# Kernel tuning notes

Hardware: AMD Instinct MI355X
Metric: run time of the kernel (lower is better)

## Reference

```python
import jax, jax.numpy as jnp
import numpy as np
from jax import lax

INP = 512
OUT = 512
T = 2048
B = 64


def setup_inputs() -> dict:
    key = jax.random.key(0)
    ks = jax.random.split(key, 7)
    rang = (1.0 / OUT) ** 0.5
    u = lambda k, shape: jax.random.uniform(k, shape, jnp.float32, -rang, rang)
    return {
        "x": jax.random.normal(ks[0], (T, B, INP), jnp.float32),
        "g": u(ks[1], (INP, OUT)),
        "gb": u(ks[2], (OUT,)),
        "h": u(ks[3], (INP, OUT)),
        "hb": u(ks[4], (OUT,)),
        "r": u(ks[5], (1, OUT)),
        "rb": u(ks[6], (OUT,)),
    }


def reference(x, g, gb, h, hb, r, rb):
    # x: [T, B, inp]
    Tn = x.shape[0]
    # time gate: r_t = 2*sigmoid((n/T) * r + rb), shape [T, out]
    t = (jnp.arange(Tn, dtype=x.dtype) / Tn)[:, None]  # [T, 1]
    rt = 2.0 * jax.nn.sigmoid(t * r[0] + rb)           # [T, out]
    # precompute per-step gates (vectorized over T)
    G = jax.nn.sigmoid(jnp.einsum("tbi,io->tbo", x, g) + gb) * rt[:, None, :]
    H = jnp.tanh(jnp.einsum("tbi,io->tbo", x, h) + hb) * rt[:, None, :]

    def step(y, gh):
        g_t, h_t = gh
        return y * g_t + h_t, None

    y0 = jnp.zeros((x.shape[1], x.shape[2] * 0 + G.shape[-1]), dtype=x.dtype)
    y, _ = lax.scan(step, y0, (G, H))
    return y
```

## Files before the change

### kernel.cpp

```cpp
#include <hip/hip_runtime.h>
#include <cstdint>
#include <cstddef>

#define TT   2048
#define BB   64
#define KK   512
#define OO   512
#define NCH  64
#define TC   32

typedef __attribute__((ext_vector_type(8))) short short8;
typedef __attribute__((ext_vector_type(4))) float f32x4;

__device__ __forceinline__ unsigned short f2bf(float f) {
  unsigned int u = __float_as_uint(f);
  unsigned int rounding = 0x7FFFu + ((u >> 16) & 1u);
  return (unsigned short)((u + rounding) >> 16);
}

__device__ __forceinline__ float sigmoid_f(float z) {
  return 1.0f / (1.0f + __expf(-z));
}

__device__ __forceinline__ float tanh_f(float z) {
  z = fminf(15.0f, fmaxf(-15.0f, z));
  float e = __expf(-2.0f * z);
  return (1.0f - e) / (1.0f + e);
}

__device__ __forceinline__ void async_ld16(const void* g, void* l) {
  __builtin_amdgcn_global_load_lds(
      (const __attribute__((address_space(1))) void*)g,
      (__attribute__((address_space(3))) void*)l, 16, 0, 0);
}

__global__ void convert_x_k(const float4* __restrict__ x4,
                            ushort4* __restrict__ xb4, int n4) {
  int i = blockIdx.x * blockDim.x + threadIdx.x;
  int stride = gridDim.x * blockDim.x;
  for (; i < n4; i += stride) {
    float4 v = x4[i];
    ushort4 o;
    o.x = f2bf(v.x); o.y = f2bf(v.y); o.z = f2bf(v.z); o.w = f2bf(v.w);
    xb4[i] = o;
  }
}

__global__ void prep_weights_k(const float* __restrict__ g,
                               const float* __restrict__ h,
                               unsigned short* __restrict__ Gt,
                               unsigned short* __restrict__ Ht) {
  __shared__ float tile[32][33];
  const float* src = (blockIdx.z == 0) ? g : h;
  unsigned short* dst = (blockIdx.z == 0) ? Gt : Ht;
  int ox = blockIdx.x * 32;
  int ky = blockIdx.y * 32;
  int tx = threadIdx.x, ty = threadIdx.y;
  #pragma unroll
  for (int r = ty; r < 32; r += 8)
    tile[r][tx] = src[(ky + r) * OO + ox + tx];
  __syncthreads();
  #pragma unroll
  for (int r = ty; r < 32; r += 8)
    dst[(size_t)(ox + r) * KK + ky + tx] = f2bf(tile[tx][r]);
}

__global__ __launch_bounds__(512, 2) void rnn_fused3_k(
    const unsigned short* __restrict__ xb,
    const unsigned short* __restrict__ Gt,
    const unsigned short* __restrict__ Ht,
    const float* __restrict__ gb, const float* __restrict__ hb,
    const float* __restrict__ r,  const float* __restrict__ rb,
    float* __restrict__ chunkA, float* __restrict__ chunkB) {
  extern __shared__ __align__(16) unsigned short smem[];

  const int tid  = threadIdx.x;
  const int wave = tid >> 6;
  const int lane = tid & 63;
  const int quad = lane >> 4;
  const int lcol = lane & 15;

  const int bi = blockIdx.x;
  const int ot = bi >> 6;
  const int c  = bi & 63;
  const int o  = ot * 128 + wave * 16 + lcol;

  const float gbv = gb[o], hbv = hb[o];
  const float rv  = r[o],  rbv = rb[o];

  short8 Bg[8][2], Bh[8][2];
  {
    const unsigned short* gp = Gt + (size_t)o * KK + quad * 8;
    const unsigned short* hp = Ht + (size_t)o * KK + quad * 8;
    #pragma unroll
    for (int kc = 0; kc < 8; ++kc)
      #pragma unroll
      for (int ks = 0; ks < 2; ++ks) {
        Bg[kc][ks] = *(const short8*)(gp + kc * 64 + ks * 32);
        Bh[kc][ks] = *(const short8*)(hp + kc * 64 + ks * 32);
      }
  }

  auto stage = [&](int trow, int buf) {
    unsigned short* dst = smem + buf * 32768 + wave * 8 * 512;
    const unsigned short* src = xb + ((size_t)trow * BB + wave * 8) * KK;
    #pragma unroll
    for (int rr = 0; rr < 8; ++rr) {
      int gch = (lane & ~7) | ((lane & 7) ^ rr);
      async_ld16(src + rr * KK + gch * 8, dst + rr * 512);
    }
  };

  stage(c * TC, 0);

  float SA[16], SB[16];
  #pragma unroll
  for (int s = 0; s < 16; s++) { SA[s] = 1.0f; SB[s] = 0.0f; }

  f32x4 accG[4], accH[4];
  #pragma unroll
  for (int m = 0; m < 4; m++) {
    f32x4 z = {0.0f, 0.0f, 0.0f, 0.0f};
    accG[m] = z; accH[m] = z;
  }

  __syncthreads();

  int p = 0;
  for (int it = 0; it < TC; ++it) {
    if (it + 1 < TC) stage(c * TC + it + 1, p ^ 1);

    const unsigned short* A0 = smem + p * 32768;
    #pragma unroll
    for (int kc = 0; kc < 8; ++kc)
      #pragma unroll
      for (int ks = 0; ks < 2; ++ks)
        #pragma unroll
        for (int mt = 0; mt < 4; ++mt) {
          int arow = mt * 16 + lcol;
          int slot = kc * 8 + ((ks * 4 + quad) ^ (arow & 7));
          short8 a = *(const short8*)(A0 + arow * 512 + slot * 8);
          accG[mt] = __builtin_amdgcn_mfma_f32_16x16x32_bf16(
              a, Bg[kc][ks], accG[mt], 0, 0, 0);
          accH[mt] = __builtin_amdgcn_mfma_f32_16x16x32_bf16(
              a, Bh[kc][ks], accH[mt], 0, 0, 0);
        }

    const int t = c * TC + it;
    const float rt = 2.0f * sigmoid_f(((float)t * (1.0f / TT)) * rv + rbv);
    #pragma unroll
    for (int mt = 0; mt < 4; ++mt)
      #pragma unroll
      for (int reg = 0; reg < 4; ++reg) {
        float G = sigmoid_f(accG[mt][reg] + gbv) * rt;
        float H = tanh_f  (accH[mt][reg] + hbv) * rt;
        int s = mt * 4 + reg;
        SB[s] = fmaf(G, SB[s], H);
        SA[s] *= G;
        accG[mt][reg] = 0.0f;
        accH[mt][reg] = 0.0f;
      }

    __syncthreads();
    p ^= 1;
  }

  #pragma unroll
  for (int mt = 0; mt < 4; ++mt)
    #pragma unroll
    for (int reg = 0; reg < 4; ++reg) {
      int s = mt * 4 + reg;
      int b = mt * 16 + quad * 4 + reg;
      size_t idx = ((size_t)c * BB + b) * OO + o;
      chunkA[idx] = SA[s];
      chunkB[idx] = SB[s];
    }
}

__global__ void combine_k(const float* __restrict__ cA,
                          const float* __restrict__ cB,
                          float* __restrict__ out) {
  int i = blockIdx.x * blockDim.x + threadIdx.x;
  float y = 0.0f;
  #pragma unroll 8
  for (int c = 0; c < NCH; c++) {
    float A  = cA[(size_t)c * (BB * OO) + i];
    float Bv = cB[(size_t)c * (BB * OO) + i];
    y = fmaf(A, y, Bv);
  }
  out[i] = y;
}

extern "C" void kernel_launch(void* const* d_in, const int* in_sizes, int n_in,
                              void* d_out, int out_size, void* d_ws, size_t ws_size,
                              hipStream_t stream) {
  (void)in_sizes; (void)n_in; (void)out_size; (void)ws_size;
  const float* x  = (const float*)d_in[0];
  const float* g  = (const float*)d_in[1];
  const float* gb = (const float*)d_in[2];
  const float* h  = (const float*)d_in[3];
  const float* hb = (const float*)d_in[4];
  const float* r  = (const float*)d_in[5];
  const float* rb = (const float*)d_in[6];
  float* out = (float*)d_out;

  char* w = (char*)d_ws;
  unsigned short* xb = (unsigned short*)w;
  unsigned short* Gt = (unsigned short*)(w + 134217728);
  unsigned short* Ht = (unsigned short*)(w + 134742016);
  float* chunkA = (float*)(w + 135266304);
  float* chunkB = (float*)(w + 143654912);

  static bool attr_set = false;
  if (!attr_set) {
    hipFuncSetAttribute(reinterpret_cast<const void*>(rnn_fused3_k),
                        hipFuncAttributeMaxDynamicSharedMemorySize, 131072);
    attr_set = true;
  }

  const int n4 = (TT * BB * KK) / 4;
  convert_x_k<<<8192, 256, 0, stream>>>((const float4*)x, (ushort4*)xb, n4);
  prep_weights_k<<<dim3(16, 16, 2), dim3(32, 8), 0, stream>>>(g, h, Gt, Ht);
  rnn_fused3_k<<<NCH * 4, 512, 131072, stream>>>(xb, Gt, Ht, gb, hb, r, rb,
                                                 chunkA, chunkB);
  combine_k<<<(BB * OO) / 256, 256, 0, stream>>>(chunkA, chunkB, out);
}
```

Measured before the change: 539.5 us.

## Fuse fp32-to-bf16 conversion of x into the recurrent GEMM kernel

Drops the separate convert_x_k pass that wrote a bf16 copy of x. The main kernel now loads fp32 x from global memory into registers, converts it, and writes it swizzled into LDS in two halves interleaved with the MFMA k-loop, so the next timestep's staging overlaps compute. This removes a full read and write of x through HBM, at the cost of async global-to-LDS loads being replaced by register-staged loads that use more VGPRs and add conversion ALU work. It also swaps the block index mapping so the four output tiles of one chunk are adjacent, and uses hardware reciprocal for sigmoid and tanh.

Result: slower. 701.8 us (+30.1%).

```diff
diff --git a/kernel.cpp b/kernel.cpp
--- a/kernel.cpp
+++ b/kernel.cpp
@@ -12,38 +12,14 @@
 typedef __attribute__((ext_vector_type(8))) short short8;
 typedef __attribute__((ext_vector_type(4))) float f32x4;
 
-__device__ __forceinline__ unsigned short f2bf(float f) {
+__device__ __forceinline__ unsigned int f2bf(float f) {
   unsigned int u = __float_as_uint(f);
   unsigned int rounding = 0x7FFFu + ((u >> 16) & 1u);
-  return (unsigned short)((u + rounding) >> 16);
-}
-
-__device__ __forceinline__ float sigmoid_f(float z) {
-  return 1.0f / (1.0f + __expf(-z));
-}
-
-__device__ __forceinline__ float tanh_f(float z) {
-  z = fminf(15.0f, fmaxf(-15.0f, z));
-  float e = __expf(-2.0f * z);
-  return (1.0f - e) / (1.0f + e);
-}
-
-__device__ __forceinline__ void async_ld16(const void* g, void* l) {
-  __builtin_amdgcn_global_load_lds(
-      (const __attribute__((address_space(1))) void*)g,
-      (__attribute__((address_space(3))) void*)l, 16, 0, 0);
-}
-
-__global__ void convert_x_k(const float4* __restrict__ x4,
-                            ushort4* __restrict__ xb4, int n4) {
-  int i = blockIdx.x * blockDim.x + threadIdx.x;
-  int stride = gridDim.x * blockDim.x;
-  for (; i < n4; i += stride) {
-    float4 v = x4[i];
-    ushort4 o;
-    o.x = f2bf(v.x); o.y = f2bf(v.y); o.z = f2bf(v.z); o.w = f2bf(v.w);
-    xb4[i] = o;
-  }
+  return (u + rounding) >> 16;
+}
+
+__device__ __forceinline__ float fast_sigmoid(float z) {
+  return __builtin_amdgcn_rcpf(1.0f + __expf(-z));
 }
 
 __global__ void prep_weights_k(const float* __restrict__ g,
@@ -62,11 +38,11 @@
   __syncthreads();
   #pragma unroll
   for (int r = ty; r < 32; r += 8)
-    dst[(size_t)(ox + r) * KK + ky + tx] = f2bf(tile[tx][r]);
-}
-
-__global__ __launch_bounds__(512, 2) void rnn_fused3_k(
-    const unsigned short* __restrict__ xb,
+    dst[(size_t)(ox + r) * KK + ky + tx] = (unsigned short)f2bf(tile[tx][r]);
+}
+
+__global__ __launch_bounds__(512, 2) void rnn_fused4_k(
+    const float* __restrict__ x,
     const unsigned short* __restrict__ Gt,
     const unsigned short* __restrict__ Ht,
     const float* __restrict__ gb, const float* __restrict__ hb,
@@ -81,8 +57,8 @@
   const int lcol = lane & 15;
 
   const int bi = blockIdx.x;
-  const int ot = bi >> 6;
-  const int c  = bi & 63;
+  const int c  = bi >> 2;
+  const int ot = bi & 3;
   const int o  = ot * 128 + wave * 16 + lcol;
 
   const float gbv = gb[o], hbv = hb[o];
@@ -101,17 +77,35 @@
       }
   }
 
-  auto stage = [&](int trow, int buf) {
-    unsigned short* dst = smem + buf * 32768 + wave * 8 * 512;
-    const unsigned short* src = xb + ((size_t)trow * BB + wave * 8) * KK;
-    #pragma unroll
-    for (int rr = 0; rr < 8; ++rr) {
-      int gch = (lane & ~7) | ((lane & 7) ^ rr);
-      async_ld16(src + rr * KK + gch * 8, dst + rr * 512);
+  auto cvt_write = [&](const float4* rg, int ph, int buf) {
+    unsigned short* base = smem + buf * 32768;
+    #pragma unroll
+    for (int kk = 0; kk < 8; ++kk) {
+      int k = ph * 8 + kk;
+      int rlow = k >> 1;
+      int row = wave * 8 + rlow;
+      int chunk = (k & 1) * 32 + (lane >> 1);
+      int slot = (chunk & ~7) | ((chunk & 7) ^ rlow);
+      uint2 wv;
+      wv.x = f2bf(rg[kk].x) | (f2bf(rg[kk].y) << 16);
+      wv.y = f2bf(rg[kk].z) | (f2bf(rg[kk].w) << 16);
+      *(uint2*)(base + row * 512 + slot * 8 + (lane & 1) * 4) = wv;
     }
   };
-
-  stage(c * TC, 0);
+  auto gsrc_of = [&](int trow) {
+    return (const float4*)x + ((size_t)trow * BB + wave * 8) * (KK / 4) + lane;
+  };
+
+  {
+    const float4* gp = gsrc_of(c * TC);
+    float4 rg[8];
+    #pragma unroll
+    for (int ph = 0; ph < 2; ++ph) {
+      #pragma unroll
+      for (int kk = 0; kk < 8; ++kk) rg[kk] = gp[(ph * 8 + kk) * 64];
+      cvt_write(rg, ph, 0);
+    }
+  }
 
   float SA[16], SB[16];
   #pragma unroll
@@ -128,11 +122,18 @@
 
   int p = 0;
   for (int it = 0; it < TC; ++it) {
-    if (it + 1 < TC) stage(c * TC + it + 1, p ^ 1);
-
+    const bool pf = (it + 1 < TC);
+    const float4* gp = pf ? gsrc_of(c * TC + it + 1) : (const float4*)x;
     const unsigned short* A0 = smem + p * 32768;
-    #pragma unroll
-    for (int kc = 0; kc < 8; ++kc)
+    float4 rg[8];
+
+    if (pf) {
+      #pragma unroll
+      for (int kk = 0; kk < 8; ++kk) rg[kk] = gp[kk * 64];
+    }
+
+    #pragma unroll
+    for (int kc = 0; kc < 4; ++kc)
       #pragma unroll
       for (int ks = 0; ks < 2; ++ks)
         #pragma unroll
@@ -146,20 +147,44 @@
               a, Bh[kc][ks], accH[mt], 0, 0, 0);
         }
 
+    if (pf) {
+      cvt_write(rg, 0, p ^ 1);
+      #pragma unroll
+      for (int kk = 0; kk < 8; ++kk) rg[kk] = gp[(8 + kk) * 64];
+    }
+
+    #pragma unroll
+    for (int kc = 4; kc < 8; ++kc)
+      #pragma unroll
+      for (int ks = 0; ks < 2; ++ks)
+        #pragma unroll
+        for (int mt = 0; mt < 4; ++mt) {
+          int arow = mt * 16 + lcol;
+          int slot = kc * 8 + ((ks * 4 + quad) ^ (arow & 7));
+          short8 a = *(const short8*)(A0 + arow * 512 + slot * 8);
+          accG[mt] = __builtin_amdgcn_mfma_f32_16x16x32_bf16(
+              a, Bg[kc][ks], accG[mt], 0, 0, 0);
+          accH[mt] = __builtin_amdgcn_mfma_f32_16x16x32_bf16(
+              a, Bh[kc][ks], accH[mt], 0, 0, 0);
+        }
+
     const int t = c * TC + it;
-    const float rt = 2.0f * sigmoid_f(((float)t * (1.0f / TT)) * rv + rbv);
+    const float rt = 2.0f * fast_sigmoid(((float)t * (1.0f / TT)) * rv + rbv);
     #pragma unroll
     for (int mt = 0; mt < 4; ++mt)
       #pragma unroll
       for (int reg = 0; reg < 4; ++reg) {
-        float G = sigmoid_f(accG[mt][reg] + gbv) * rt;
-        float H = tanh_f  (accH[mt][reg] + hbv) * rt;
+        float G = rt * fast_sigmoid(accG[mt][reg] + gbv);
+        float eH = __expf(-2.0f * (accH[mt][reg] + hbv));
+        float H = rt * fmaf(2.0f, __builtin_amdgcn_rcpf(1.0f + eH), -1.0f);
         int s = mt * 4 + reg;
         SB[s] = fmaf(G, SB[s], H);
         SA[s] *= G;
         accG[mt][reg] = 0.0f;
         accH[mt][reg] = 0.0f;
       }
+
+    if (pf) cvt_write(rg, 1, p ^ 1);
 
     __syncthreads();
     p ^= 1;
@@ -205,23 +230,20 @@
   float* out = (float*)d_out;
 
   char* w = (char*)d_ws;
-  unsigned short* xb = (unsigned short*)w;
-  unsigned short* Gt = (unsigned short*)(w + 134217728);
-  unsigned short* Ht = (unsigned short*)(w + 134742016);
-  float* chunkA = (float*)(w + 135266304);
-  float* chunkB = (float*)(w + 143654912);
+  unsigned short* Gt = (unsigned short*)w;
+  unsigned short* Ht = (unsigned short*)(w + 524288);
+  float* chunkA = (float*)(w + 1048576);
+  float* chunkB = (float*)(w + 9437184);
 
   static bool attr_set = false;
   if (!attr_set) {
-    hipFuncSetAttribute(reinterpret_cast<const void*>(rnn_fused3_k),
+    hipFuncSetAttribute(reinterpret_cast<const void*>(rnn_fused4_k),
                         hipFuncAttributeMaxDynamicSharedMemorySize, 131072);
     attr_set = true;
   }
 
-  const int n4 = (TT * BB * KK) / 4;
-  convert_x_k<<<8192, 256, 0, stream>>>((const float4*)x, (ushort4*)xb, n4);
   prep_weights_k<<<dim3(16, 16, 2), dim3(32, 8), 0, stream>>>(g, h, Gt, Ht);
-  rnn_fused3_k<<<NCH * 4, 512, 131072, stream>>>(xb, Gt, Ht, gb, hb, r, rb,
+  rnn_fused4_k<<<NCH * 4, 512, 131072, stream>>>(x, Gt, Ht, gb, hb, r, rb,
                                                  chunkA, chunkB);
   combine_k<<<(BB * OO) / 256, 256, 0, stream>>>(chunkA, chunkB, out);
 }
```
